# Kernel optimization log

Hardware: AMD Instinct MI355X
Metric: run time of the kernel (lower is better)

## Reference

```python
import jax, jax.numpy as jnp
import numpy as np

B, S, D = 2, 2048, 1024
H, DH = 16, 64
LN_EPS = 1e-5
NEG_INF = -1e9


def setup_inputs() -> dict:
    key = jax.random.key(0)
    ks = jax.random.split(key, 8)
    x = jax.random.normal(ks[0], (B, S, D), dtype=jnp.float32)
    mask = jax.random.randint(ks[1], (B, 1, S, S), 0, 5) == 0
    sc = 1.0 / np.sqrt(D)
    W_attn = jax.random.normal(ks[2], (D, 3 * H * DH), dtype=jnp.float32) * sc
    b_attn = jnp.zeros((3 * H * DH,), dtype=jnp.float32)
    W_out = jax.random.normal(ks[3], (H * DH, D), dtype=jnp.float32) * sc
    b_out = jnp.zeros((D,), dtype=jnp.float32)
    ln_g = jnp.ones((D,), dtype=jnp.float32)
    ln_b = jnp.zeros((D,), dtype=jnp.float32)
    return {"x": x, "W_attn": W_attn, "b_attn": b_attn, "W_out": W_out,
            "b_out": b_out, "ln_g": ln_g, "ln_b": ln_b, "mask": mask}


def reference(x, W_attn, b_attn, W_out, b_out, ln_g, ln_b, mask):
    bs, s, _ = x.shape
    qkv = x @ W_attn + b_attn                      # [b, s, 3*H*DH]
    q, k, v = jnp.split(qkv, 3, axis=-1)
    q = q.reshape(bs, s, H, DH)
    k = k.reshape(bs, s, H, DH)
    v = v.reshape(bs, s, H, DH)
    scores = jnp.einsum('bqhd,bkhd->bhqk', q, k) / np.sqrt(DH)
    scores = jnp.where(mask, NEG_INF, scores)
    probs = jax.nn.softmax(scores, axis=-1)        # attn_p = 0 -> dropout is identity
    attn = jnp.einsum('bhqk,bkhd->bqhd', probs, v).reshape(bs, s, H * DH)
    y = x + (attn @ W_out + b_out)                 # resid_p = 0
    mu = jnp.mean(y, axis=-1, keepdims=True)
    var = jnp.mean((y - mu) ** 2, axis=-1, keepdims=True)
    return (y - mu) * jax.lax.rsqrt(var + LN_EPS) * ln_g + ln_b
```

## Files before the change

### kernel.cpp

```cpp
#include <hip/hip_runtime.h>
#include <math.h>

#define BB 2
#define SS 2048
#define DD 1024
#define HH 16
#define DHD 64
#define N3 3072
#define LN_EPS 1e-5f

#define PLANE (BB*HH*SS*DHD)

typedef __attribute__((ext_vector_type(8))) short bf16x8;
typedef __attribute__((ext_vector_type(4))) float f32x4;
typedef unsigned int u32;
typedef unsigned short ushort_t;

static __device__ __forceinline__ short f2bf(float f) {
  union { float f; unsigned u; } a;
  a.f = f;
  unsigned r = a.u + 0x7fffu + ((a.u >> 16) & 1u);
  return (short)(r >> 16);
}

static __device__ __forceinline__ short f2bf_rhu(float f) {
  union { float f; unsigned u; } a;
  a.f = f;
  return (short)((a.u + 0x8000u) >> 16);
}

static __device__ __forceinline__ void gload_lds16(const void* g, void* l) {
  __builtin_amdgcn_global_load_lds(
      (const __attribute__((address_space(1))) u32*)g,
      (__attribute__((address_space(3))) u32*)l, 16, 0, 0);
}

__global__ __launch_bounds__(256) void conv_bf16_kernel(
    const float* __restrict__ in, ushort_t* __restrict__ out) {
  int i = (blockIdx.x * 256 + threadIdx.x) * 8;
  float4 a = *(const float4*)&in[i];
  float4 b = *(const float4*)&in[i + 4];
  short s[8] = {f2bf(a.x), f2bf(a.y), f2bf(a.z), f2bf(a.w),
                f2bf(b.x), f2bf(b.y), f2bf(b.z), f2bf(b.w)};
  *(bf16x8*)&out[i] = *(bf16x8*)s;
}

__global__ __launch_bounds__(256) void transpose_bf16_kernel(
    const float* __restrict__ W, ushort_t* __restrict__ Wt, int K, int N) {
  __shared__ float tile[64][65];
  const int tid = threadIdx.x;
  const int nb = blockIdx.x * 64, kb = blockIdx.y * 64;
  #pragma unroll
  for (int i = 0; i < 4; ++i) {
    int idx = tid + i * 256;
    int r = idx >> 4, c = (idx & 15) * 4;
    float4 v = *(const float4*)&W[(size_t)(kb + r) * N + nb + c];
    tile[r][c] = v.x; tile[r][c + 1] = v.y; tile[r][c + 2] = v.z; tile[r][c + 3] = v.w;
  }
  __syncthreads();
  #pragma unroll
  for (int i = 0; i < 4; ++i) {
    int idx = tid + i * 256;
    int n = idx >> 4, k = (idx & 15) * 4;
    short4 s;
    s.x = f2bf(tile[k][n]); s.y = f2bf(tile[k + 1][n]);
    s.z = f2bf(tile[k + 2][n]); s.w = f2bf(tile[k + 3][n]);
    *(short4*)&Wt[(size_t)(nb + n) * K + kb + k] = s;
  }
}

__global__ __launch_bounds__(256) void pack_mask_kernel(
    const int* __restrict__ mask, unsigned long long* __restrict__ bits) {
  size_t g = (size_t)blockIdx.x * 256 + threadIdx.x;
  int m = mask[g];
  unsigned long long b = __ballot(m != 0);
  if ((threadIdx.x & 63) == 0) bits[g >> 6] = b;
}

#define GEMM_MAIN(Aptr, Btptr, Kdim)                                          \
  __shared__ ushort_t As[128 * 64];                                           \
  __shared__ ushort_t Bs[128 * 64];                                           \
  const int tid = threadIdx.x;                                                \
  const int wave = tid >> 6, lane = tid & 63;                                 \
  const int lane16 = lane & 15, quad = lane >> 4;                             \
  const int wm = wave & 1, wn = wave >> 1;                                    \
  const int bm = blockIdx.y * 128, bn = blockIdx.x * 128;                     \
  const int srow = lane >> 3;                                                 \
  const int sg = (lane & 7) ^ srow;                                           \
  f32x4 acc[4][4];                                                            \
  _Pragma("unroll") for (int i = 0; i < 4; ++i)                               \
    _Pragma("unroll") for (int j = 0; j < 4; ++j)                             \
      acc[i][j] = (f32x4){0.f, 0.f, 0.f, 0.f};                                \
  const ushort_t* agp[4];                                                     \
  const ushort_t* bgp[4];                                                     \
  _Pragma("unroll") for (int i = 0; i < 4; ++i) {                             \
    int seg = wave * 4 + i;                                                   \
    int r = seg * 8 + srow;                                                   \
    agp[i] = Aptr + (size_t)(bm + r) * Kdim + sg * 8;                         \
    bgp[i] = Btptr + (size_t)(bn + r) * Kdim + sg * 8;                        \
  }                                                                           \
  for (int k0 = 0; k0 < Kdim; k0 += 64) {                                     \
    _Pragma("unroll") for (int i = 0; i < 4; ++i) {                           \
      int seg = wave * 4 + i;                                                 \
      gload_lds16(agp[i] + k0, &As[seg * 512]);                               \
      gload_lds16(bgp[i] + k0, &Bs[seg * 512]);                               \
    }                                                                         \
    __syncthreads();                                                          \
    _Pragma("unroll") for (int ks = 0; ks < 2; ++ks) {                        \
      bf16x8 af[4], bfr[4];                                                   \
      _Pragma("unroll") for (int mt = 0; mt < 4; ++mt) {                      \
        int ra = wm * 64 + mt * 16 + lane16;                                  \
        int kc = ks * 4 + quad;                                               \
        af[mt] = *(const bf16x8*)&As[ra * 64 + ((kc ^ (ra & 7)) * 8)];        \
      }                                                                       \
      _Pragma("unroll") for (int nt = 0; nt < 4; ++nt) {                      \
        int rb = wn * 64 + nt * 16 + lane16;                                  \
        int kc = ks * 4 + quad;                                               \
        bfr[nt] = *(const bf16x8*)&Bs[rb * 64 + ((kc ^ (rb & 7)) * 8)];       \
      }                                                                       \
      _Pragma("unroll") for (int mt = 0; mt < 4; ++mt)                        \
        _Pragma("unroll") for (int nt = 0; nt < 4; ++nt)                      \
          acc[mt][nt] = __builtin_amdgcn_mfma_f32_16x16x32_bf16(              \
              af[mt], bfr[nt], acc[mt][nt], 0, 0, 0);                         \
    }                                                                         \
    __syncthreads();                                                          \
  }

__global__ __launch_bounds__(256) void gemm_qkv_mfma(
    const ushort_t* __restrict__ A, const ushort_t* __restrict__ Bt,
    const float* __restrict__ bias, ushort_t* __restrict__ qkvh) {
  GEMM_MAIN(A, Bt, DD)
  #pragma unroll
  for (int nt = 0; nt < 4; ++nt) {
    int col = bn + wn * 64 + nt * 16 + lane16;
    int which = col >> 10, hcol = col & 1023;
    int head = hcol >> 6, d = hcol & 63;
    float bv = bias[col];
    ushort_t* plane = qkvh + (size_t)which * PLANE;
    #pragma unroll
    for (int mt = 0; mt < 4; ++mt) {
      #pragma unroll
      for (int reg = 0; reg < 4; ++reg) {
        int row = bm + wm * 64 + mt * 16 + quad * 4 + reg;
        int bb = row >> 11, ss = row & (SS - 1);
        plane[((size_t)(bb * HH + head) * SS + ss) * DHD + d] =
            (ushort_t)f2bf(acc[mt][nt][reg] + bv);
      }
    }
  }
}

__global__ __launch_bounds__(256) void gemm_proj_mfma(
    const ushort_t* __restrict__ A, const ushort_t* __restrict__ Bt,
    const float* __restrict__ bias, const float* __restrict__ xres,
    float* __restrict__ Y) {
  GEMM_MAIN(A, Bt, DD)
  #pragma unroll
  for (int nt = 0; nt < 4; ++nt) {
    int col = bn + wn * 64 + nt * 16 + lane16;
    float bv = bias[col];
    #pragma unroll
    for (int mt = 0; mt < 4; ++mt) {
      #pragma unroll
      for (int reg = 0; reg < 4; ++reg) {
        int row = bm + wm * 64 + mt * 16 + quad * 4 + reg;
        Y[(size_t)row * DD + col] =
            acc[mt][nt][reg] + bv + xres[(size_t)row * DD + col];
      }
    }
  }
}

__global__ __launch_bounds__(512) void attn_mfma_kernel(
    const ushort_t* __restrict__ qh, const ushort_t* __restrict__ kh,
    const ushort_t* __restrict__ vh, const u32* __restrict__ mbits,
    ushort_t* __restrict__ attn_out) {
  __shared__ __align__(16) short Kt[64][76];
  __shared__ __align__(16) short Vt[64][76];
  __shared__ __align__(16) short Pt[8][16][76];

  const int tid = threadIdx.x;
  const int wave = tid >> 6, lane = tid & 63;
  const int lane16 = lane & 15, quad = lane >> 4;

  const int bh = blockIdx.x & 31;
  const int qt = blockIdx.x >> 5;
  const int bbi = bh >> 4, hhi = bh & 15;
  const size_t head_base = (size_t)bh * SS * DHD;
  const int q0 = qt * 128 + wave * 16;
  const int qrow_g = q0 + quad * 4;

  bf16x8 qf[2];
  {
    const float kScale = 0.125f * 1.44269504f;
    const ushort_t* qsrc = &qh[head_base + (size_t)(q0 + lane16) * DHD + quad * 8];
    #pragma unroll
    for (int ks = 0; ks < 2; ++ks) {
      bf16x8 r = *(const bf16x8*)&qsrc[ks * 32];
      #pragma unroll
      for (int e = 0; e < 8; ++e) {
        union { u32 u; float f; } c;
        c.u = ((u32)(ushort_t)r[e]) << 16;
        c.f *= kScale;
        r[e] = f2bf(c.f);
      }
      qf[ks] = r;
    }
  }

  bf16x8 onesf;
  #pragma unroll
  for (int e = 0; e < 8; ++e) onesf[e] = (short)0x3F80;

  f32x4 acc[4];
  f32x4 lacc = (f32x4){0.f, 0.f, 0.f, 0.f};
  #pragma unroll
  for (int dt = 0; dt < 4; ++dt) acc[dt] = (f32x4){0.f, 0.f, 0.f, 0.f};

  const u32* mrow_base = mbits + ((size_t)(bbi * SS) + qrow_g) * 64;

  const int kg_r = tid >> 3;
  const int kg_c = (tid & 7) * 8;
  const int vs_c = tid & 63;
  const int vs_rb = (tid >> 6) * 8;

  bf16x8 kreg;
  short4 vreg[2];
  uint2 mwn[4];
  {
    kreg = *(const bf16x8*)&kh[head_base + (size_t)kg_r * DHD + kg_c];
    #pragma unroll
    for (int i = 0; i < 2; ++i) {
      int r0 = vs_rb + i * 4;
      const ushort_t* vsrc = &vh[head_base + (size_t)r0 * DHD + vs_c];
      vreg[i].x = (short)vsrc[0];
      vreg[i].y = (short)vsrc[DHD];
      vreg[i].z = (short)vsrc[2 * DHD];
      vreg[i].w = (short)vsrc[3 * DHD];
    }
    #pragma unroll
    for (int reg = 0; reg < 4; ++reg)
      mwn[reg] = *(const uint2*)&mrow_base[(size_t)reg * 64];
  }

  for (int kt = 0; kt < SS; kt += 64) {
    __syncthreads();
    *(bf16x8*)&Kt[kg_r][kg_c] = kreg;
    #pragma unroll
    for (int i = 0; i < 2; ++i)
      *(short4*)&Vt[vs_c][vs_rb + i * 4] = vreg[i];
    uint2 mwc[4];
    #pragma unroll
    for (int reg = 0; reg < 4; ++reg) mwc[reg] = mwn[reg];
    __syncthreads();

    const int kt2 = kt + 64;
    if (kt2 < SS) {
      kreg = *(const bf16x8*)&kh[head_base + (size_t)(kt2 + kg_r) * DHD + kg_c];
      #pragma unroll
      for (int i = 0; i < 2; ++i) {
        int r0 = kt2 + vs_rb + i * 4;
        const ushort_t* vsrc = &vh[head_base + (size_t)r0 * DHD + vs_c];
        vreg[i].x = (short)vsrc[0];
        vreg[i].y = (short)vsrc[DHD];
        vreg[i].z = (short)vsrc[2 * DHD];
        vreg[i].w = (short)vsrc[3 * DHD];
      }
      #pragma unroll
      for (int reg = 0; reg < 4; ++reg)
        mwn[reg] = *(const uint2*)&mrow_base[(size_t)reg * 64 + (kt2 >> 5)];
    }

    f32x4 sc[4];
    #pragma unroll
    for (int nt = 0; nt < 4; ++nt) {
      sc[nt] = (f32x4){0.f, 0.f, 0.f, 0.f};
      #pragma unroll
      for (int ks = 0; ks < 2; ++ks) {
        bf16x8 kf = *(const bf16x8*)&Kt[nt * 16 + lane16][ks * 32 + quad * 8];
        sc[nt] = __builtin_amdgcn_mfma_f32_16x16x32_bf16(qf[ks], kf, sc[nt], 0, 0, 0);
      }
    }

    #pragma unroll
    for (int reg = 0; reg < 4; ++reg) {
      u32 tl = mwc[reg].x >> lane16;
      u32 th = mwc[reg].y >> lane16;
      float e0 = (tl & 1u)       ? 0.f : exp2f(sc[0][reg]);
      float e1 = (tl & 0x10000u) ? 0.f : exp2f(sc[1][reg]);
      float e2 = (th & 1u)       ? 0.f : exp2f(sc[2][reg]);
      float e3 = (th & 0x10000u) ? 0.f : exp2f(sc[3][reg]);
      Pt[wave][quad * 4 + reg][ 0 + lane16] = f2bf_rhu(e0);
      Pt[wave][quad * 4 + reg][16 + lane16] = f2bf_rhu(e1);
      Pt[wave][quad * 4 + reg][32 + lane16] = f2bf_rhu(e2);
      Pt[wave][quad * 4 + reg][48 + lane16] = f2bf_rhu(e3);
    }

    #pragma unroll
    for (int ks = 0; ks < 2; ++ks) {
      bf16x8 pf = *(const bf16x8*)&Pt[wave][lane16][ks * 32 + quad * 8];
      lacc = __builtin_amdgcn_mfma_f32_16x16x32_bf16(pf, onesf, lacc, 0, 0, 0);
      #pragma unroll
      for (int dt = 0; dt < 4; ++dt) {
        bf16x8 vf = *(const bf16x8*)&Vt[dt * 16 + lane16][ks * 32 + quad * 8];
        acc[dt] = __builtin_amdgcn_mfma_f32_16x16x32_bf16(pf, vf, acc[dt], 0, 0, 0);
      }
    }
  }

  #pragma unroll
  for (int reg = 0; reg < 4; ++reg) {
    float inv = 1.0f / lacc[reg];
    ushort_t* orow = &attn_out[((size_t)(bbi * SS) + qrow_g + reg) * DD
                               + hhi * DHD + lane16];
    #pragma unroll
    for (int dt = 0; dt < 4; ++dt)
      orow[dt * 16] = (ushort_t)f2bf(acc[dt][reg] * inv);
  }
}

__global__ __launch_bounds__(256) void ln_kernel(
    float* __restrict__ Y, const float* __restrict__ g,
    const float* __restrict__ bta) {
  const int r = blockIdx.x;
  const int tid = threadIdx.x;
  float4 v = *(const float4*)&Y[(size_t)r * DD + tid * 4];
  float sum = v.x + v.y + v.z + v.w;
  float sq = v.x * v.x + v.y * v.y + v.z * v.z + v.w * v.w;
  #pragma unroll
  for (int off = 32; off; off >>= 1) {
    sum += __shfl_down(sum, off);
    sq += __shfl_down(sq, off);
  }
  __shared__ float ps[4], pq[4];
  __shared__ float mu_s, rs_s;
  const int wave = tid >> 6;
  if ((tid & 63) == 0) { ps[wave] = sum; pq[wave] = sq; }
  __syncthreads();
  if (tid == 0) {
    float s = ps[0] + ps[1] + ps[2] + ps[3];
    float qq = pq[0] + pq[1] + pq[2] + pq[3];
    float mu = s * (1.0f / DD);
    float var = qq * (1.0f / DD) - mu * mu;
    mu_s = mu;
    rs_s = rsqrtf(var + LN_EPS);
  }
  __syncthreads();
  const float mu = mu_s, rs = rs_s;
  float4 g4 = *(const float4*)&g[tid * 4];
  float4 b4 = *(const float4*)&bta[tid * 4];
  float4 ov;
  ov.x = (v.x - mu) * rs * g4.x + b4.x;
  ov.y = (v.y - mu) * rs * g4.y + b4.y;
  ov.z = (v.z - mu) * rs * g4.z + b4.z;
  ov.w = (v.w - mu) * rs * g4.w + b4.w;
  *(float4*)&Y[(size_t)r * DD + tid * 4] = ov;
}

extern "C" void kernel_launch(void* const* d_in, const int* in_sizes, int n_in,
                              void* d_out, int out_size, void* d_ws, size_t ws_size,
                              hipStream_t stream) {
  const float* x      = (const float*)d_in[0];
  const float* W_attn = (const float*)d_in[1];
  const float* b_attn = (const float*)d_in[2];
  const float* W_out  = (const float*)d_in[3];
  const float* b_out  = (const float*)d_in[4];
  const float* ln_g   = (const float*)d_in[5];
  const float* ln_b   = (const float*)d_in[6];
  const int*   mask   = (const int*)d_in[7];
  float* out = (float*)d_out;
  ushort_t* ws = (ushort_t*)d_ws;

  ushort_t* xb    = ws;
  ushort_t* watt  = xb + (size_t)BB * SS * DD;
  ushort_t* wot   = watt + (size_t)N3 * DD;
  ushort_t* qh    = wot + (size_t)DD * DD;
  ushort_t* kh    = qh + (size_t)PLANE;
  ushort_t* vh    = kh + (size_t)PLANE;
  ushort_t* attnb = vh + (size_t)PLANE;
  u32* mbits      = (u32*)(attnb + (size_t)BB * SS * DD);

  conv_bf16_kernel<<<dim3((BB * SS * DD) / (256 * 8)), 256, 0, stream>>>(x, xb);
  transpose_bf16_kernel<<<dim3(N3 / 64, DD / 64), 256, 0, stream>>>(W_attn, watt, DD, N3);
  transpose_bf16_kernel<<<dim3(DD / 64, DD / 64), 256, 0, stream>>>(W_out, wot, DD, DD);
  pack_mask_kernel<<<dim3((BB * SS * SS) / 256), 256, 0, stream>>>(
      mask, (unsigned long long*)mbits);

  gemm_qkv_mfma<<<dim3(N3 / 128, (BB * SS) / 128), 256, 0, stream>>>(
      xb, watt, b_attn, qh);
  attn_mfma_kernel<<<dim3(BB * HH * (SS / 128)), 512, 0, stream>>>(
      qh, kh, vh, mbits, attnb);
  gemm_proj_mfma<<<dim3(DD / 128, (BB * SS) / 128), 256, 0, stream>>>(
      attnb, wot, b_out, x, out);
  ln_kernel<<<dim3(BB * SS), 256, 0, stream>>>(out, ln_g, ln_b);
}
```

Measured before the change: 270.8 us.

## Merge preprocessing kernels and process 128-key tiles per attention sync

```diff
diff --git a/kernel.cpp b/kernel.cpp
--- a/kernel.cpp
+++ b/kernel.cpp
@@ -35,46 +35,67 @@
       (__attribute__((address_space(3))) u32*)l, 16, 0, 0);
 }
 
-__global__ __launch_bounds__(256) void conv_bf16_kernel(
-    const float* __restrict__ in, ushort_t* __restrict__ out) {
-  int i = (blockIdx.x * 256 + threadIdx.x) * 8;
-  float4 a = *(const float4*)&in[i];
-  float4 b = *(const float4*)&in[i + 4];
-  short s[8] = {f2bf(a.x), f2bf(a.y), f2bf(a.z), f2bf(a.w),
-                f2bf(b.x), f2bf(b.y), f2bf(b.z), f2bf(b.w)};
-  *(bf16x8*)&out[i] = *(bf16x8*)s;
-}
-
-__global__ __launch_bounds__(256) void transpose_bf16_kernel(
-    const float* __restrict__ W, ushort_t* __restrict__ Wt, int K, int N) {
+#define PREP_CONV_B   2048
+#define PREP_TA_B     768
+#define PREP_TO_B     256
+#define PREP_PACK_B   32768
+#define PREP_TOTAL_B  (PREP_CONV_B + PREP_TA_B + PREP_TO_B + PREP_PACK_B)
+
+__global__ __launch_bounds__(256) void prep_kernel(
+    const float* __restrict__ x, ushort_t* __restrict__ xb,
+    const float* __restrict__ Wa, ushort_t* __restrict__ watt,
+    const float* __restrict__ Wo, ushort_t* __restrict__ wot,
+    const int* __restrict__ mask, unsigned long long* __restrict__ bits) {
   __shared__ float tile[64][65];
   const int tid = threadIdx.x;
-  const int nb = blockIdx.x * 64, kb = blockIdx.y * 64;
-  #pragma unroll
-  for (int i = 0; i < 4; ++i) {
-    int idx = tid + i * 256;
-    int r = idx >> 4, c = (idx & 15) * 4;
-    float4 v = *(const float4*)&W[(size_t)(kb + r) * N + nb + c];
-    tile[r][c] = v.x; tile[r][c + 1] = v.y; tile[r][c + 2] = v.z; tile[r][c + 3] = v.w;
-  }
-  __syncthreads();
-  #pragma unroll
-  for (int i = 0; i < 4; ++i) {
-    int idx = tid + i * 256;
-    int n = idx >> 4, k = (idx & 15) * 4;
-    short4 s;
-    s.x = f2bf(tile[k][n]); s.y = f2bf(tile[k + 1][n]);
-    s.z = f2bf(tile[k + 2][n]); s.w = f2bf(tile[k + 3][n]);
-    *(short4*)&Wt[(size_t)(nb + n) * K + kb + k] = s;
-  }
-}
-
-__global__ __launch_bounds__(256) void pack_mask_kernel(
-    const int* __restrict__ mask, unsigned long long* __restrict__ bits) {
-  size_t g = (size_t)blockIdx.x * 256 + threadIdx.x;
-  int m = mask[g];
-  unsigned long long b = __ballot(m != 0);
-  if ((threadIdx.x & 63) == 0) bits[g >> 6] = b;
+  const int bid = blockIdx.x;
+
+  if (bid < PREP_CONV_B) {
+    int i = (bid * 256 + tid) * 8;
+    float4 a = *(const float4*)&x[i];
+    float4 b = *(const float4*)&x[i + 4];
+    short s[8] = {f2bf(a.x), f2bf(a.y), f2bf(a.z), f2bf(a.w),
+                  f2bf(b.x), f2bf(b.y), f2bf(b.z), f2bf(b.w)};
+    *(bf16x8*)&xb[i] = *(bf16x8*)s;
+    return;
+  }
+  if (bid < PREP_CONV_B + PREP_TA_B + PREP_TO_B) {
+    const float* W; ushort_t* Wt; int K, N, nb, kb;
+    if (bid < PREP_CONV_B + PREP_TA_B) {
+      int idx = bid - PREP_CONV_B;
+      W = Wa; Wt = watt; K = DD; N = N3;
+      nb = (idx % 48) * 64; kb = (idx / 48) * 64;
+    } else {
+      int idx = bid - PREP_CONV_B - PREP_TA_B;
+      W = Wo; Wt = wot; K = DD; N = DD;
+      nb = (idx % 16) * 64; kb = (idx / 16) * 64;
+    }
+    #pragma unroll
+    for (int i = 0; i < 4; ++i) {
+      int idx = tid + i * 256;
+      int r = idx >> 4, c = (idx & 15) * 4;
+      float4 v = *(const float4*)&W[(size_t)(kb + r) * N + nb + c];
+      tile[r][c] = v.x; tile[r][c + 1] = v.y;
+      tile[r][c + 2] = v.z; tile[r][c + 3] = v.w;
+    }
+    __syncthreads();
+    #pragma unroll
+    for (int i = 0; i < 4; ++i) {
+      int idx = tid + i * 256;
+      int n = idx >> 4, k = (idx & 15) * 4;
+      short4 s;
+      s.x = f2bf(tile[k][n]); s.y = f2bf(tile[k + 1][n]);
+      s.z = f2bf(tile[k + 2][n]); s.w = f2bf(tile[k + 3][n]);
+      *(short4*)&Wt[(size_t)(nb + n) * K + kb + k] = s;
+    }
+    return;
+  }
+  {
+    size_t g = (size_t)(bid - PREP_CONV_B - PREP_TA_B - PREP_TO_B) * 256 + tid;
+    int m = mask[g];
+    unsigned long long b = __ballot(m != 0);
+    if ((tid & 63) == 0) bits[g >> 6] = b;
+  }
 }
 
 #define GEMM_MAIN(Aptr, Btptr, Kdim)                                          \
@@ -175,8 +196,8 @@
     const ushort_t* __restrict__ qh, const ushort_t* __restrict__ kh,
     const ushort_t* __restrict__ vh, const u32* __restrict__ mbits,
     ushort_t* __restrict__ attn_out) {
-  __shared__ __align__(16) short Kt[64][76];
-  __shared__ __align__(16) short Vt[64][76];
+  __shared__ __align__(16) short Kt[2][64][76];
+  __shared__ __align__(16) short Vt[2][64][76];
   __shared__ __align__(16) short Pt[8][16][76];
 
   const int tid = threadIdx.x;
@@ -222,16 +243,20 @@
   const int kg_r = tid >> 3;
   const int kg_c = (tid & 7) * 8;
   const int vs_c = tid & 63;
-  const int vs_rb = (tid >> 6) * 8;
-
-  bf16x8 kreg;
-  short4 vreg[2];
-  uint2 mwn[4];
+  const int v_half = wave >> 2;
+  const int vs_rb_l = (wave & 3) * 16;
+  const int vs_rb_g = wave * 16;
+
+  bf16x8 kreg[2];
+  short4 vreg[4];
+  uint4 mwn[4];
   {
-    kreg = *(const bf16x8*)&kh[head_base + (size_t)kg_r * DHD + kg_c];
-    #pragma unroll
-    for (int i = 0; i < 2; ++i) {
-      int r0 = vs_rb + i * 4;
+    #pragma unroll
+    for (int i = 0; i < 2; ++i)
+      kreg[i] = *(const bf16x8*)&kh[head_base + (size_t)(kg_r + i * 64) * DHD + kg_c];
+    #pragma unroll
+    for (int i = 0; i < 4; ++i) {
+      int r0 = vs_rb_g + i * 4;
       const ushort_t* vsrc = &vh[head_base + (size_t)r0 * DHD + vs_c];
       vreg[i].x = (short)vsrc[0];
       vreg[i].y = (short)vsrc[DHD];
@@ -240,26 +265,30 @@
     }
     #pragma unroll
     for (int reg = 0; reg < 4; ++reg)
-      mwn[reg] = *(const uint2*)&mrow_base[(size_t)reg * 64];
-  }
-
-  for (int kt = 0; kt < SS; kt += 64) {
+      mwn[reg] = *(const uint4*)&mrow_base[(size_t)reg * 64];
+  }
+
+  for (int kt = 0; kt < SS; kt += 128) {
     __syncthreads();
-    *(bf16x8*)&Kt[kg_r][kg_c] = kreg;
     #pragma unroll
     for (int i = 0; i < 2; ++i)
-      *(short4*)&Vt[vs_c][vs_rb + i * 4] = vreg[i];
-    uint2 mwc[4];
+      *(bf16x8*)&Kt[i][kg_r][kg_c] = kreg[i];
+    #pragma unroll
+    for (int i = 0; i < 4; ++i)
+      *(short4*)&Vt[v_half][vs_c][vs_rb_l + i * 4] = vreg[i];
+    uint4 mwc[4];
     #pragma unroll
     for (int reg = 0; reg < 4; ++reg) mwc[reg] = mwn[reg];
     __syncthreads();
 
-    const int kt2 = kt + 64;
+    const int kt2 = kt + 128;
     if (kt2 < SS) {
-      kreg = *(const bf16x8*)&kh[head_base + (size_t)(kt2 + kg_r) * DHD + kg_c];
-      #pragma unroll
-      for (int i = 0; i < 2; ++i) {
-        int r0 = kt2 + vs_rb + i * 4;
+      #pragma unroll
+      for (int i = 0; i < 2; ++i)
+        kreg[i] = *(const bf16x8*)&kh[head_base + (size_t)(kt2 + kg_r + i * 64) * DHD + kg_c];
+      #pragma unroll
+      for (int i = 0; i < 4; ++i) {
+        int r0 = kt2 + vs_rb_g + i * 4;
         const ushort_t* vsrc = &vh[head_base + (size_t)r0 * DHD + vs_c];
         vreg[i].x = (short)vsrc[0];
         vreg[i].y = (short)vsrc[DHD];
@@ -268,42 +297,45 @@
       }
       #pragma unroll
       for (int reg = 0; reg < 4; ++reg)
-        mwn[reg] = *(const uint2*)&mrow_base[(size_t)reg * 64 + (kt2 >> 5)];
-    }
-
-    f32x4 sc[4];
-    #pragma unroll
-    for (int nt = 0; nt < 4; ++nt) {
-      sc[nt] = (f32x4){0.f, 0.f, 0.f, 0.f};
+        mwn[reg] = *(const uint4*)&mrow_base[(size_t)reg * 64 + (kt2 >> 5)];
+    }
+
+    #pragma unroll
+    for (int h = 0; h < 2; ++h) {
+      f32x4 sc[4];
+      #pragma unroll
+      for (int nt = 0; nt < 4; ++nt) {
+        sc[nt] = (f32x4){0.f, 0.f, 0.f, 0.f};
+        #pragma unroll
+        for (int ks = 0; ks < 2; ++ks) {
+          bf16x8 kf = *(const bf16x8*)&Kt[h][nt * 16 + lane16][ks * 32 + quad * 8];
+          sc[nt] = __builtin_amdgcn_mfma_f32_16x16x32_bf16(qf[ks], kf, sc[nt], 0, 0, 0);
+        }
+      }
+
+      #pragma unroll
+      for (int reg = 0; reg < 4; ++reg) {
+        u32 tl = (h ? mwc[reg].z : mwc[reg].x) >> lane16;
+        u32 th = (h ? mwc[reg].w : mwc[reg].y) >> lane16;
+        float e0 = (tl & 1u)       ? 0.f : exp2f(sc[0][reg]);
+        float e1 = (tl & 0x10000u) ? 0.f : exp2f(sc[1][reg]);
+        float e2 = (th & 1u)       ? 0.f : exp2f(sc[2][reg]);
+        float e3 = (th & 0x10000u) ? 0.f : exp2f(sc[3][reg]);
+        Pt[wave][quad * 4 + reg][ 0 + lane16] = f2bf_rhu(e0);
+        Pt[wave][quad * 4 + reg][16 + lane16] = f2bf_rhu(e1);
+        Pt[wave][quad * 4 + reg][32 + lane16] = f2bf_rhu(e2);
+        Pt[wave][quad * 4 + reg][48 + lane16] = f2bf_rhu(e3);
+      }
+
       #pragma unroll
       for (int ks = 0; ks < 2; ++ks) {
-        bf16x8 kf = *(const bf16x8*)&Kt[nt * 16 + lane16][ks * 32 + quad * 8];
-        sc[nt] = __builtin_amdgcn_mfma_f32_16x16x32_bf16(qf[ks], kf, sc[nt], 0, 0, 0);
-      }
-    }
-
-    #pragma unroll
-    for (int reg = 0; reg < 4; ++reg) {
-      u32 tl = mwc[reg].x >> lane16;
-      u32 th = mwc[reg].y >> lane16;
-      float e0 = (tl & 1u)       ? 0.f : exp2f(sc[0][reg]);
-      float e1 = (tl & 0x10000u) ? 0.f : exp2f(sc[1][reg]);
-      float e2 = (th & 1u)       ? 0.f : exp2f(sc[2][reg]);
-      float e3 = (th & 0x10000u) ? 0.f : exp2f(sc[3][reg]);
-      Pt[wave][quad * 4 + reg][ 0 + lane16] = f2bf_rhu(e0);
-      Pt[wave][quad * 4 + reg][16 + lane16] = f2bf_rhu(e1);
-      Pt[wave][quad * 4 + reg][32 + lane16] = f2bf_rhu(e2);
-      Pt[wave][quad * 4 + reg][48 + lane16] = f2bf_rhu(e3);
-    }
-
-    #pragma unroll
-    for (int ks = 0; ks < 2; ++ks) {
-      bf16x8 pf = *(const bf16x8*)&Pt[wave][lane16][ks * 32 + quad * 8];
-      lacc = __builtin_amdgcn_mfma_f32_16x16x32_bf16(pf, onesf, lacc, 0, 0, 0);
-      #pragma unroll
-      for (int dt = 0; dt < 4; ++dt) {
-        bf16x8 vf = *(const bf16x8*)&Vt[dt * 16 + lane16][ks * 32 + quad * 8];
-        acc[dt] = __builtin_amdgcn_mfma_f32_16x16x32_bf16(pf, vf, acc[dt], 0, 0, 0);
+        bf16x8 pf = *(const bf16x8*)&Pt[wave][lane16][ks * 32 + quad * 8];
+        lacc = __builtin_amdgcn_mfma_f32_16x16x32_bf16(pf, onesf, lacc, 0, 0, 0);
+        #pragma unroll
+        for (int dt = 0; dt < 4; ++dt) {
+          bf16x8 vf = *(const bf16x8*)&Vt[h][dt * 16 + lane16][ks * 32 + quad * 8];
+          acc[dt] = __builtin_amdgcn_mfma_f32_16x16x32_bf16(pf, vf, acc[dt], 0, 0, 0);
+        }
       }
     }
   }
@@ -380,11 +412,8 @@
   ushort_t* attnb = vh + (size_t)PLANE;
   u32* mbits      = (u32*)(attnb + (size_t)BB * SS * DD);
 
-  conv_bf16_kernel<<<dim3((BB * SS * DD) / (256 * 8)), 256, 0, stream>>>(x, xb);
-  transpose_bf16_kernel<<<dim3(N3 / 64, DD / 64), 256, 0, stream>>>(W_attn, watt, DD, N3);
-  transpose_bf16_kernel<<<dim3(DD / 64, DD / 64), 256, 0, stream>>>(W_out, wot, DD, DD);
-  pack_mask_kernel<<<dim3((BB * SS * SS) / 256), 256, 0, stream>>>(
-      mask, (unsigned long long*)mbits);
+  prep_kernel<<<dim3(PREP_TOTAL_B), 256, 0, stream>>>(
+      x, xb, W_attn, watt, W_out, wot, mask, (unsigned long long*)mbits);
 
   gemm_qkv_mfma<<<dim3(N3 / 128, (BB * SS) / 128), 256, 0, stream>>>(
       xb, watt, b_attn, qh);
```

Result: no change. 266.5 us (-1.6%).
